# Optimization experiments

Hardware: AMD Instinct MI355X
Metric: run time of the kernel (lower is better)

Reference implementation:

```python
import jax, jax.numpy as jnp
import numpy as np

N = 100000   # nodes
E = 600000   # edges
B = 512      # graphs in batch
H = 128      # hidden dim
ED = 8       # edge feature dim
TWO48 = float(2 ** 48 - 1)


def _w(k, shape, fan_in):
    return jax.random.normal(k, shape, jnp.float32) * (1.0 / np.sqrt(fan_in))


def setup_inputs() -> dict:
    key = jax.random.key(0)
    ks = jax.random.split(key, 32)
    inp = {}
    inp["s_node_ids"] = jax.random.randint(ks[0], (N,), 0, 2 ** 31 - 1, dtype=jnp.int32)
    inp["s_edge_index"] = jax.random.randint(ks[1], (2, E), 0, N, dtype=jnp.int32)
    inp["s_edge_attr"] = jax.random.normal(ks[2], (E, ED), jnp.float32)
    inp["s_batch"] = jnp.sort(jax.random.randint(ks[3], (N,), 0, B, dtype=jnp.int32))
    inp["depth"] = jax.random.uniform(ks[4], (B,), jnp.float32)
    # id_mlp: Linear(1,H) -> ReLU -> Linear(H,H)
    inp["id_w1"] = _w(ks[5], (1, H), 1); inp["id_b1"] = jnp.zeros((H,), jnp.float32)
    inp["id_w2"] = _w(ks[6], (H, H), H); inp["id_b2"] = jnp.zeros((H,), jnp.float32)
    # edge_mlp: Linear(ED,H) -> ReLU -> Linear(H,H)
    inp["ed_w1"] = _w(ks[7], (ED, H), ED); inp["ed_b1"] = jnp.zeros((H,), jnp.float32)
    inp["ed_w2"] = _w(ks[8], (H, H), H); inp["ed_b2"] = jnp.zeros((H,), jnp.float32)
    # GINEConv nn MLPs: Linear(H,H) -> ReLU -> Linear(H,H)
    inp["c1_w1"] = _w(ks[9], (H, H), H); inp["c1_b1"] = jnp.zeros((H,), jnp.float32)
    inp["c1_w2"] = _w(ks[10], (H, H), H); inp["c1_b2"] = jnp.zeros((H,), jnp.float32)
    inp["c2_w1"] = _w(ks[11], (H, H), H); inp["c2_b1"] = jnp.zeros((H,), jnp.float32)
    inp["c2_w2"] = _w(ks[12], (H, H), H); inp["c2_b2"] = jnp.zeros((H,), jnp.float32)
    inp["rg_w1"] = _w(ks[13], (H + 1, H), H + 1); inp["rg_b1"] = jnp.zeros((H,), jnp.float32)
    inp["rg_w2"] = _w(ks[14], (H, 1), H); inp["rg_b2"] = jnp.zeros((1,), jnp.float32)
    return inp


def _mlp2(x, w1, b1, w2, b2):
    return jax.nn.relu(x @ w1 + b1) @ w2 + b2


def _gine(x, src, dst, e, w1, b1, w2, b2):
    # message = ReLU(x_j + e), sum-aggregated at dst; out = nn((1+eps)*x + aggr), eps=0
    msg = jax.nn.relu(x[src] + e)                       # [E, H]
    aggr = jax.ops.segment_sum(msg, dst, num_segments=N)  # [N, H]
    return _mlp2(x + aggr, w1, b1, w2, b2)


def _global_mean(x, batch):
    sums = jax.ops.segment_sum(x, batch, num_segments=B)                          # [B, H]
    cnts = jax.ops.segment_sum(jnp.ones((x.shape[0], 1), x.dtype), batch, num_segments=B)
    return sums / jnp.maximum(cnts, 1.0)


def reference(s_node_ids, s_edge_index, s_edge_attr, s_batch, depth,
              id_w1, id_b1, id_w2, id_b2,
              ed_w1, ed_b1, ed_w2, ed_b2,
              c1_w1, c1_b1, c1_w2, c1_b2,
              c2_w1, c2_b1, c2_w2, c2_b2,
              rg_w1, rg_b1, rg_w2, rg_b2):
    src, dst = s_edge_index[0], s_edge_index[1]
    x0 = jnp.clip(s_node_ids.astype(jnp.float32) / TWO48, 0.0, 1.0)[:, None]  # [N,1]
    x = _mlp2(x0, id_w1, id_b1, id_w2, id_b2)                                 # [N,H]
    e = _mlp2(s_edge_attr, ed_w1, ed_b1, ed_w2, ed_b2)                        # [E,H]
    x = jax.nn.relu(_gine(x, src, dst, e, c1_w1, c1_b1, c1_w2, c1_b2))
    x = jax.nn.relu(_gine(x, src, dst, e, c2_w1, c2_b1, c2_w2, c2_b2))
    rep = jnp.concatenate([_global_mean(x, s_batch), depth[:, None]], axis=1)  # [B,H+1]
    return _mlp2(rep, rg_w1, rg_b1, rg_w2, rg_b2)[:, 0]                        # [B]
```

## Files before the change

### kernel.cpp

```cpp
#include <hip/hip_runtime.h>
#include <hip/hip_bf16.h>

#define N_NODES 100000
#define N_EDGES 600000
#define NB      512
#define H       128
#define ED      8
#define SCAN_CHUNK 1024
#define N_CHUNKS   98

typedef __attribute__((ext_vector_type(8))) short short8;
typedef __attribute__((ext_vector_type(4))) float f32x4;
typedef __attribute__((ext_vector_type(4))) unsigned int u32x4;
typedef unsigned short u16;
typedef unsigned int   u32;

static __device__ __forceinline__ u16 f2bf(float f) {
    u32 u = __float_as_uint(f);
    u32 r = u + 0x7fffu + ((u >> 16) & 1u);
    return (u16)(r >> 16);
}
static __device__ __forceinline__ float bf2f(u32 h) {
    return __uint_as_float(h << 16);
}

__global__ __launch_bounds__(256) void pack_all_kernel(
    const float* __restrict__ W0, const float* __restrict__ W1,
    const float* __restrict__ W2, const float* __restrict__ W3,
    const float* __restrict__ W4, const float* __restrict__ W5,
    const float* __restrict__ W6,
    short8* __restrict__ O0, short8* __restrict__ O1,
    short8* __restrict__ O2, short8* __restrict__ O3,
    short8* __restrict__ O4, short8* __restrict__ O5,
    short8* __restrict__ O6)
{
    int gid = blockIdx.x * 256 + threadIdx.x;
    const int total = 512 + 6 * 2048;
    if (gid >= total) return;
    const float* W; short8* O; int Krows, kkmax, slot;
    if (gid < 512) { W = W0; O = O0; Krows = ED; kkmax = 1; slot = gid; }
    else {
        int m = (gid - 512) / 2048;
        slot = (gid - 512) % 2048;
        Krows = H; kkmax = 4;
        switch (m) {
            case 0: W = W1; O = O1; break;
            case 1: W = W2; O = O2; break;
            case 2: W = W3; O = O3; break;
            case 3: W = W4; O = O4; break;
            case 4: W = W5; O = O5; break;
            default: W = W6; O = O6; break;
        }
    }
    int lane = slot & 63;
    int t = slot >> 6;
    int nt = t & 1; t >>= 1;
    int kk = t % kkmax;
    int w  = t / kkmax;
    int quad = lane >> 4, n15 = lane & 15;
    int n = w * 32 + nt * 16 + n15;
    short8 v;
    #pragma unroll
    for (int j = 0; j < 8; j++) {
        int k = kk * 32 + quad * 8 + j;
        v[j] = (k < Krows) ? (short)f2bf(W[k * H + n]) : (short)0;
    }
    O[slot] = v;
}

__global__ __launch_bounds__(256) void hist_kernel(
    const int* __restrict__ edge_index, int* __restrict__ counts)
{
    int e = blockIdx.x * 256 + threadIdx.x;
    if (e < N_EDGES) atomicAdd(&counts[edge_index[N_EDGES + e]], 1);
}

__global__ __launch_bounds__(SCAN_CHUNK) void scan1_kernel(
    const int* __restrict__ counts, int* __restrict__ chunk_scan,
    int* __restrict__ bsum_raw)
{
    __shared__ int s[SCAN_CHUNK];
    int tid = threadIdx.x;
    int gid = blockIdx.x * SCAN_CHUNK + tid;
    int v = counts[gid];
    s[tid] = v;
    __syncthreads();
    #pragma unroll
    for (int off = 1; off < SCAN_CHUNK; off <<= 1) {
        int t = (tid >= off) ? s[tid - off] : 0;
        __syncthreads();
        s[tid] += t;
        __syncthreads();
    }
    chunk_scan[gid] = s[tid] - v;
    if (tid == SCAN_CHUNK - 1) bsum_raw[blockIdx.x] = s[tid];
}

__global__ __launch_bounds__(128) void scan2_kernel(
    const int* __restrict__ bsum_raw, int* __restrict__ bsum_scan)
{
    __shared__ int s[128];
    int tid = threadIdx.x;
    int v = (tid < N_CHUNKS) ? bsum_raw[tid] : 0;
    s[tid] = v;
    __syncthreads();
    #pragma unroll
    for (int off = 1; off < 128; off <<= 1) {
        int t = (tid >= off) ? s[tid - off] : 0;
        __syncthreads();
        s[tid] += t;
        __syncthreads();
    }
    bsum_scan[tid] = s[tid] - v;
}

__global__ __launch_bounds__(256) void fill_kernel(
    const int* __restrict__ edge_index,
    const int* __restrict__ chunk_scan, const int* __restrict__ bsum_scan,
    int* __restrict__ counts, int* __restrict__ src_list,
    int* __restrict__ pos_of)
{
    int e = blockIdx.x * 256 + threadIdx.x;
    if (e >= N_EDGES) return;
    int src = edge_index[e];
    int dst = edge_index[N_EDGES + e];
    int slot = atomicAdd(&counts[dst], -1) - 1;
    int pos = chunk_scan[dst] + bsum_scan[dst >> 10] + slot;
    src_list[pos] = src;
    pos_of[e] = pos;
}

__global__ __launch_bounds__(256) void finalize_offsets(
    const int* __restrict__ chunk_scan, const int* __restrict__ bsum_scan,
    int* __restrict__ row_start)
{
    int i = blockIdx.x * 256 + threadIdx.x;
    if (i <= N_NODES) row_start[i] = chunk_scan[i] + bsum_scan[i >> 10];
}

__global__ __launch_bounds__(256) void node_mlp_mfma(
    const int* __restrict__ ids,
    const float* __restrict__ w1, const float* __restrict__ b1,
    const short8* __restrict__ pW2, const float* __restrict__ b2,
    u16* __restrict__ x_out)
{
    __shared__ u16 sH[64 * 136];
    __shared__ float s_x0[64];
    int tid = threadIdx.x;
    int w = tid >> 6, lane = tid & 63, quad = lane >> 4, n15 = lane & 15;
    short8 fW2[4][2];
    #pragma unroll
    for (int kk = 0; kk < 4; kk++) {
        fW2[kk][0] = pW2[((w * 4 + kk) * 2 + 0) * 64 + lane];
        fW2[kk][1] = pW2[((w * 4 + kk) * 2 + 1) * 64 + lane];
    }
    float rb2[2] = { b2[w * 32 + n15], b2[w * 32 + 16 + n15] };
    float w1c = w1[tid & 127], b1c = b1[tid & 127];
    const int ntile = (N_NODES + 63) / 64;
    for (int tile = blockIdx.x; tile < ntile; tile += gridDim.x) {
        int row0 = tile * 64;
        if (tid < 64) {
            int n = row0 + tid;
            float x0 = (n < N_NODES) ? (float)ids[n] / 281474976710655.0f : 0.0f;
            s_x0[tid] = fminf(fmaxf(x0, 0.0f), 1.0f);
        }
        __syncthreads();
        int half = tid >> 7, c = tid & 127;
        #pragma unroll 8
        for (int rr = 0; rr < 32; rr++) {
            int r = half + rr * 2;
            sH[r * 136 + c] = f2bf(fmaxf(s_x0[r] * w1c + b1c, 0.0f));
        }
        __syncthreads();
        f32x4 acc[4][2];
        #pragma unroll
        for (int s = 0; s < 4; s++) { acc[s][0] = (f32x4){0,0,0,0}; acc[s][1] = (f32x4){0,0,0,0}; }
        #pragma unroll
        for (int kk = 0; kk < 4; kk++) {
            #pragma unroll
            for (int s = 0; s < 4; s++) {
                short8 a = *(const short8*)&sH[(s * 16 + n15) * 136 + kk * 32 + quad * 8];
                acc[s][0] = __builtin_amdgcn_mfma_f32_16x16x32_bf16(a, fW2[kk][0], acc[s][0], 0, 0, 0);
                acc[s][1] = __builtin_amdgcn_mfma_f32_16x16x32_bf16(a, fW2[kk][1], acc[s][1], 0, 0, 0);
            }
        }
        __syncthreads();
        #pragma unroll
        for (int s = 0; s < 4; s++)
            #pragma unroll
            for (int nt = 0; nt < 2; nt++) {
                int col = w * 32 + nt * 16 + n15;
                #pragma unroll
                for (int reg = 0; reg < 4; reg++)
                    sH[(s * 16 + quad * 4 + reg) * 136 + col] =
                        f2bf(acc[s][nt][reg] + rb2[nt]);
            }
        __syncthreads();
        for (int idx = tid; idx < 64 * 16; idx += 256) {
            int r = idx >> 4, c8 = (idx & 15) << 3;
            int n = row0 + r;
            if (n < N_NODES)
                *(uint4*)&x_out[(long)n * H + c8] = *(const uint4*)&sH[r * 136 + c8];
        }
        __syncthreads();
    }
}

__global__ __launch_bounds__(256) void edge_mlp_mfma(
    const float* __restrict__ attr,
    const int* __restrict__ pos_of,
    const short8* __restrict__ pW1, const float* __restrict__ b1,
    const short8* __restrict__ pW2, const float* __restrict__ b2,
    u16* __restrict__ e_perm)
{
    __shared__ u16 sA[64 * 40];
    __shared__ u16 sH[64 * 136];
    __shared__ int sPos[64];
    int tid = threadIdx.x;
    int w = tid >> 6, lane = tid & 63, quad = lane >> 4, n15 = lane & 15;
    short8 fW1[2];
    fW1[0] = pW1[(w * 2 + 0) * 64 + lane];
    fW1[1] = pW1[(w * 2 + 1) * 64 + lane];
    short8 fW2[4][2];
    #pragma unroll
    for (int kk = 0; kk < 4; kk++) {
        fW2[kk][0] = pW2[((w * 4 + kk) * 2 + 0) * 64 + lane];
        fW2[kk][1] = pW2[((w * 4 + kk) * 2 + 1) * 64 + lane];
    }
    float rb1[2] = { b1[w * 32 + n15], b1[w * 32 + 16 + n15] };
    float rb2[2] = { b2[w * 32 + n15], b2[w * 32 + 16 + n15] };
    const int ntile = N_EDGES / 64;
    for (int tile = blockIdx.x; tile < ntile; tile += gridDim.x) {
        int row0 = tile * 64;
        if (tid < 64) sPos[tid] = pos_of[row0 + tid];
        if (tid >= 64 && tid < 192) {
            int t2 = tid - 64;
            int r = t2 >> 1, c4 = (t2 & 1) * 4;
            f32x4 v = __builtin_nontemporal_load((const f32x4*)&attr[(long)(row0 + r) * ED + c4]);
            ushort4 o;
            o.x = f2bf(v[0]); o.y = f2bf(v[1]); o.z = f2bf(v[2]); o.w = f2bf(v[3]);
            *(ushort4*)&sA[r * 40 + c4] = o;
        } else if (tid >= 192) {
            int idx = tid - 192;
            for (; idx < 192; idx += 64) {
                int r = idx / 3, c8 = 8 + (idx % 3) * 8;
                *(uint4*)&sA[r * 40 + c8] = make_uint4(0, 0, 0, 0);
            }
        }
        __syncthreads();
        f32x4 acc[4][2];
        #pragma unroll
        for (int s = 0; s < 4; s++) { acc[s][0] = (f32x4){0,0,0,0}; acc[s][1] = (f32x4){0,0,0,0}; }
        #pragma unroll
        for (int s = 0; s < 4; s++) {
            short8 a = *(const short8*)&sA[(s * 16 + n15) * 40 + quad * 8];
            acc[s][0] = __builtin_amdgcn_mfma_f32_16x16x32_bf16(a, fW1[0], acc[s][0], 0, 0, 0);
            acc[s][1] = __builtin_amdgcn_mfma_f32_16x16x32_bf16(a, fW1[1], acc[s][1], 0, 0, 0);
        }
        #pragma unroll
        for (int s = 0; s < 4; s++)
            #pragma unroll
            for (int nt = 0; nt < 2; nt++) {
                int col = w * 32 + nt * 16 + n15;
                #pragma unroll
                for (int reg = 0; reg < 4; reg++)
                    sH[(s * 16 + quad * 4 + reg) * 136 + col] =
                        f2bf(fmaxf(acc[s][nt][reg] + rb1[nt], 0.0f));
            }
        __syncthreads();
        #pragma unroll
        for (int s = 0; s < 4; s++) { acc[s][0] = (f32x4){0,0,0,0}; acc[s][1] = (f32x4){0,0,0,0}; }
        #pragma unroll
        for (int kk = 0; kk < 4; kk++) {
            #pragma unroll
            for (int s = 0; s < 4; s++) {
                short8 a = *(const short8*)&sH[(s * 16 + n15) * 136 + kk * 32 + quad * 8];
                acc[s][0] = __builtin_amdgcn_mfma_f32_16x16x32_bf16(a, fW2[kk][0], acc[s][0], 0, 0, 0);
                acc[s][1] = __builtin_amdgcn_mfma_f32_16x16x32_bf16(a, fW2[kk][1], acc[s][1], 0, 0, 0);
            }
        }
        __syncthreads();
        #pragma unroll
        for (int s = 0; s < 4; s++)
            #pragma unroll
            for (int nt = 0; nt < 2; nt++) {
                int col = w * 32 + nt * 16 + n15;
                #pragma unroll
                for (int reg = 0; reg < 4; reg++)
                    sH[(s * 16 + quad * 4 + reg) * 136 + col] =
                        f2bf(acc[s][nt][reg] + rb2[nt]);
            }
        __syncthreads();
        for (int idx = tid; idx < 64 * 16; idx += 256) {
            int r = idx >> 4, c8 = (idx & 15) << 3;
            long rr = sPos[r];
            u32x4 v = *(const u32x4*)&sH[r * 136 + c8];
            __builtin_nontemporal_store(v, (u32x4*)&e_perm[rr * H + c8]);
        }
        __syncthreads();
    }
}

static __device__ __forceinline__ void acc8(float* a, u32x4 xv, u32x4 ev) {
    #pragma unroll
    for (int q = 0; q < 4; q++) {
        a[2 * q + 0] += fmaxf(bf2f(xv[q] & 0xffff) + bf2f(ev[q] & 0xffff), 0.0f);
        a[2 * q + 1] += fmaxf(bf2f(xv[q] >> 16)    + bf2f(ev[q] >> 16),    0.0f);
    }
}

__global__ __launch_bounds__(256) void aggregate_kernel(
    const int* __restrict__ row_start,
    const int* __restrict__ src_list,
    const u16* __restrict__ e_perm,
    const u16* __restrict__ x,
    u16* __restrict__ xs_out)
{
    int tid  = threadIdx.x;
    int lane = tid & 63;
    int l16  = lane & 15;
    int base = lane & 48;
    int fo   = l16 * 8;
    int n = blockIdx.x * 16 + (tid >> 4);
    const u16* xb = x + fo;

    int beg = row_start[n];
    int end = row_start[n + 1];
    float a[8], b[8];
    #pragma unroll
    for (int q = 0; q < 8; q++) { a[q] = 0.0f; b[q] = 0.0f; }

    for (int j0 = beg; j0 < end; j0 += 16) {
        int m = min(16, end - j0);
        int sv = src_list[j0 + min(l16, m - 1)];
        const u16* ej = e_perm + (long)j0 * H + fo;
        int j = 0;
        for (; j + 2 <= m; j += 2) {
            int s0 = __shfl(sv, base | j);
            int s1 = __shfl(sv, base | (j + 1));
            u32x4 xv0 = *(const u32x4*)(xb + (long)s0 * H);
            u32x4 ev0 = __builtin_nontemporal_load((const u32x4*)(ej + (long)(j + 0) * H));
            u32x4 xv1 = *(const u32x4*)(xb + (long)s1 * H);
            u32x4 ev1 = __builtin_nontemporal_load((const u32x4*)(ej + (long)(j + 1) * H));
            acc8(a, xv0, ev0);
            acc8(b, xv1, ev1);
        }
        if (j < m) {
            int s0 = __shfl(sv, base | j);
            u32x4 xv0 = *(const u32x4*)(xb + (long)s0 * H);
            u32x4 ev0 = __builtin_nontemporal_load((const u32x4*)(ej + (long)j * H));
            acc8(a, xv0, ev0);
        }
    }
    u32x4 xself = *(const u32x4*)(xb + (long)n * H);
    u32x4 out;
    #pragma unroll
    for (int q = 0; q < 4; q++) {
        float o0 = bf2f(xself[q] & 0xffff) + a[2 * q + 0] + b[2 * q + 0];
        float o1 = bf2f(xself[q] >> 16)    + a[2 * q + 1] + b[2 * q + 1];
        out[q] = (u32)f2bf(o0) | ((u32)f2bf(o1) << 16);
    }
    __builtin_nontemporal_store(out, (u32x4*)&xs_out[(long)n * H + fo]);
}

__global__ __launch_bounds__(256) void conv_mlp_mfma(
    const u16* __restrict__ xs,
    const short8* __restrict__ pW1, const float* __restrict__ b1,
    const short8* __restrict__ pW2, const float* __restrict__ b2,
    u16* __restrict__ x_out)
{
    __shared__ u16 sA[32 * 136];
    int tid = threadIdx.x;
    int w = tid >> 6, lane = tid & 63, quad = lane >> 4, n15 = lane & 15;
    short8 fW1[4][2], fW2[4][2];
    #pragma unroll
    for (int kk = 0; kk < 4; kk++) {
        fW1[kk][0] = pW1[((w * 4 + kk) * 2 + 0) * 64 + lane];
        fW1[kk][1] = pW1[((w * 4 + kk) * 2 + 1) * 64 + lane];
        fW2[kk][0] = pW2[((w * 4 + kk) * 2 + 0) * 64 + lane];
        fW2[kk][1] = pW2[((w * 4 + kk) * 2 + 1) * 64 + lane];
    }
    float rb1[2] = { b1[w * 32 + n15], b1[w * 32 + 16 + n15] };
    float rb2[2] = { b2[w * 32 + n15], b2[w * 32 + 16 + n15] };
    const int ntile = N_NODES / 32;
    for (int tile = blockIdx.x; tile < ntile; tile += gridDim.x) {
        long row0 = (long)tile * 32;
        for (int idx = tid; idx < 32 * 16; idx += 256) {
            int r = idx >> 4, c8 = (idx & 15) << 3;
            *(uint4*)&sA[r * 136 + c8] = *(const uint4*)&xs[(row0 + r) * H + c8];
        }
        __syncthreads();
        f32x4 acc[2][2];
        #pragma unroll
        for (int s = 0; s < 2; s++) { acc[s][0] = (f32x4){0,0,0,0}; acc[s][1] = (f32x4){0,0,0,0}; }
        #pragma unroll
        for (int kk = 0; kk < 4; kk++) {
            #pragma unroll
            for (int s = 0; s < 2; s++) {
                short8 a = *(const short8*)&sA[(s * 16 + n15) * 136 + kk * 32 + quad * 8];
                acc[s][0] = __builtin_amdgcn_mfma_f32_16x16x32_bf16(a, fW1[kk][0], acc[s][0], 0, 0, 0);
                acc[s][1] = __builtin_amdgcn_mfma_f32_16x16x32_bf16(a, fW1[kk][1], acc[s][1], 0, 0, 0);
            }
        }
        __syncthreads();
        #pragma unroll
        for (int s = 0; s < 2; s++)
            #pragma unroll
            for (int nt = 0; nt < 2; nt++) {
                int col = w * 32 + nt * 16 + n15;
                #pragma unroll
                for (int reg = 0; reg < 4; reg++)
                    sA[(s * 16 + quad * 4 + reg) * 136 + col] =
                        f2bf(fmaxf(acc[s][nt][reg] + rb1[nt], 0.0f));
            }
        __syncthreads();
        #pragma unroll
        for (int s = 0; s < 2; s++) { acc[s][0] = (f32x4){0,0,0,0}; acc[s][1] = (f32x4){0,0,0,0}; }
        #pragma unroll
        for (int kk = 0; kk < 4; kk++) {
            #pragma unroll
            for (int s = 0; s < 2; s++) {
                short8 a = *(const short8*)&sA[(s * 16 + n15) * 136 + kk * 32 + quad * 8];
                acc[s][0] = __builtin_amdgcn_mfma_f32_16x16x32_bf16(a, fW2[kk][0], acc[s][0], 0, 0, 0);
                acc[s][1] = __builtin_amdgcn_mfma_f32_16x16x32_bf16(a, fW2[kk][1], acc[s][1], 0, 0, 0);
            }
        }
        __syncthreads();
        #pragma unroll
        for (int s = 0; s < 2; s++)
            #pragma unroll
            for (int nt = 0; nt < 2; nt++) {
                int col = w * 32 + nt * 16 + n15;
                #pragma unroll
                for (int reg = 0; reg < 4; reg++)
                    sA[(s * 16 + quad * 4 + reg) * 136 + col] =
                        f2bf(fmaxf(acc[s][nt][reg] + rb2[nt], 0.0f));
            }
        __syncthreads();
        for (int idx = tid; idx < 32 * 16; idx += 256) {
            int r = idx >> 4, c8 = (idx & 15) << 3;
            *(uint4*)&x_out[(row0 + r) * H + c8] = *(const uint4*)&sA[r * 136 + c8];
        }
        __syncthreads();
    }
}

__global__ __launch_bounds__(256) void pool_kernel(
    const u16* __restrict__ x, const int* __restrict__ batch,
    float* __restrict__ sums, float* __restrict__ cnt)
{
    int sg   = threadIdx.x >> 6;
    int lane = threadIdx.x & 63;
    int fo = lane * 2;
    const int nper = (N_NODES + gridDim.x - 1) / gridDim.x;
    int n0 = blockIdx.x * nper;
    int n1 = min(n0 + nper, N_NODES);
    int cur = -1;
    float a0 = 0.0f, a1 = 0.0f, c = 0.0f;
    for (int n = n0 + sg; n < n1; n += 4) {
        int b = batch[n];
        if (b != cur) {
            if (cur >= 0) {
                atomicAdd(&sums[cur * H + fo],     a0);
                atomicAdd(&sums[cur * H + fo + 1], a1);
                if (lane == 0) atomicAdd(&cnt[cur], c);
            }
            a0 = a1 = 0.0f; c = 0.0f; cur = b;
        }
        u32 xv = *(const u32*)&x[(long)n * H + fo];
        a0 += bf2f(xv & 0xffff);
        a1 += bf2f(xv >> 16);
        c += 1.0f;
    }
    if (cur >= 0) {
        atomicAdd(&sums[cur * H + fo],     a0);
        atomicAdd(&sums[cur * H + fo + 1], a1);
        if (lane == 0) atomicAdd(&cnt[cur], c);
    }
}

__global__ __launch_bounds__(128) void regressor_kernel(
    const float* __restrict__ sums, const float* __restrict__ cnt,
    const float* __restrict__ depth,
    const float* __restrict__ w1, const float* __restrict__ b1,
    const float* __restrict__ w2, const float* __restrict__ b2,
    float* __restrict__ out)
{
    __shared__ float s_mean[H];
    __shared__ float s_red[2];
    int b = blockIdx.x;
    int j = threadIdx.x;
    float c = fmaxf(cnt[b], 1.0f);
    s_mean[j] = sums[b * H + j] / c;
    __syncthreads();
    float h = b1[j];
    #pragma unroll 8
    for (int k = 0; k < H; k++) h += s_mean[k] * w1[k * H + j];
    h += depth[b] * w1[H * H + j];
    h = fmaxf(h, 0.0f);
    float p = h * w2[j];
    #pragma unroll
    for (int off = 32; off >= 1; off >>= 1) p += __shfl_down(p, off, 64);
    if ((j & 63) == 0) s_red[j >> 6] = p;
    __syncthreads();
    if (j == 0) out[b] = s_red[0] + s_red[1] + b2[0];
}

extern "C" void kernel_launch(void* const* d_in, const int* in_sizes, int n_in,
                              void* d_out, int out_size, void* d_ws, size_t ws_size,
                              hipStream_t stream)
{
    const int*   ids   = (const int*)  d_in[0];
    const int*   eidx  = (const int*)  d_in[1];
    const float* eattr = (const float*)d_in[2];
    const int*   batch = (const int*)  d_in[3];
    const float* depth = (const float*)d_in[4];
    const float* id_w1 = (const float*)d_in[5];
    const float* id_b1 = (const float*)d_in[6];
    const float* id_w2 = (const float*)d_in[7];
    const float* id_b2 = (const float*)d_in[8];
    const float* ed_w1 = (const float*)d_in[9];
    const float* ed_b1 = (const float*)d_in[10];
    const float* ed_w2 = (const float*)d_in[11];
    const float* ed_b2 = (const float*)d_in[12];
    const float* c1_w1 = (const float*)d_in[13];
    const float* c1_b1 = (const float*)d_in[14];
    const float* c1_w2 = (const float*)d_in[15];
    const float* c1_b2 = (const float*)d_in[16];
    const float* c2_w1 = (const float*)d_in[17];
    const float* c2_b1 = (const float*)d_in[18];
    const float* c2_w2 = (const float*)d_in[19];
    const float* c2_b2 = (const float*)d_in[20];
    const float* rg_w1 = (const float*)d_in[21];
    const float* rg_b1 = (const float*)d_in[22];
    const float* rg_w2 = (const float*)d_in[23];
    const float* rg_b2 = (const float*)d_in[24];

    char* ws = (char*)d_ws;
    u16*   e_buf    = (u16*)  (ws);
    u16*   x_buf    = (u16*)  (ws + 153600000);
    u16*   xs_buf   = (u16*)  (ws + 179200000);
    float* sums_buf = (float*)(ws + 204800000);
    float* cnt_buf  = (float*)(ws + 205062144);
    int*   counts   = (int*)  (ws + 205064192);
    int*   chunk_sc = (int*)  (ws + 205465600);
    int*   bsum_raw = (int*)  (ws + 205867008);
    int*   bsum_sc  = (int*)  (ws + 205867520);
    int*   src_list = (int*)  (ws + 205868032);
    int*   pos_of   = (int*)  (ws + 208268032);
    short8* ed_w1p  = (short8*)(ws + 210668032);
    short8* ed_w2p  = (short8*)(ws + 210676224);
    short8* c1_w1p  = (short8*)(ws + 210708992);
    short8* c1_w2p  = (short8*)(ws + 210741760);
    short8* c2_w1p  = (short8*)(ws + 210774528);
    short8* c2_w2p  = (short8*)(ws + 210807296);
    short8* id_w2p  = (short8*)(ws + 210840064);
    int*   row_start = counts;

    pack_all_kernel<<<50, 256, 0, stream>>>(
        ed_w1, ed_w2, c1_w1, c1_w2, c2_w1, c2_w2, id_w2,
        ed_w1p, ed_w2p, c1_w1p, c1_w2p, c2_w1p, c2_w2p, id_w2p);

    hipMemsetAsync(counts, 0, 401408, stream);
    hist_kernel <<<(N_EDGES + 255) / 256, 256, 0, stream>>>(eidx, counts);
    scan1_kernel<<<N_CHUNKS, SCAN_CHUNK, 0, stream>>>(counts, chunk_sc, bsum_raw);
    scan2_kernel<<<1, 128, 0, stream>>>(bsum_raw, bsum_sc);
    fill_kernel <<<(N_EDGES + 255) / 256, 256, 0, stream>>>(eidx, chunk_sc, bsum_sc,
                                                            counts, src_list, pos_of);
    finalize_offsets<<<(N_NODES + 256) / 256, 256, 0, stream>>>(chunk_sc, bsum_sc, row_start);

    node_mlp_mfma<<<768, 256, 0, stream>>>(ids, id_w1, id_b1, id_w2p, id_b2, x_buf);
    edge_mlp_mfma<<<2048, 256, 0, stream>>>(eattr, pos_of, ed_w1p, ed_b1, ed_w2p, ed_b2, e_buf);

    aggregate_kernel<<<6250, 256, 0, stream>>>(row_start, src_list, e_buf, x_buf, xs_buf);
    conv_mlp_mfma<<<3125, 256, 0, stream>>>(xs_buf, c1_w1p, c1_b1, c1_w2p, c1_b2, x_buf);

    aggregate_kernel<<<6250, 256, 0, stream>>>(row_start, src_list, e_buf, x_buf, xs_buf);
    conv_mlp_mfma<<<3125, 256, 0, stream>>>(xs_buf, c2_w1p, c2_b1, c2_w2p, c2_b2, x_buf);

    hipMemsetAsync(sums_buf, 0, (size_t)(NB * H + NB) * 4, stream);
    pool_kernel<<<2048, 256, 0, stream>>>(x_buf, batch, sums_buf, cnt_buf);
    regressor_kernel<<<NB, 128, 0, stream>>>(sums_buf, cnt_buf, depth,
                                             rg_w1, rg_b1, rg_w2, rg_b2, (float*)d_out);
}
```

Before: 408.1 us.

## Fuse edge MLP into GINE aggregation, recompute edge embeddings per layer

Removes the materialized 600k x 128 bf16 edge-embedding buffer. The fill kernel now writes bf16 edge attributes permuted into CSR order, and a new fused kernel recomputes the edge MLP with MFMA for each CSR chunk of 64 edges. Each block handles 32 destination nodes and accumulates relu(x_src + e) directly from LDS. This trades roughly 150MB of write-then-double-read traffic for running the edge MLP twice. It also cuts parallelism: each thread now serially walks the edges of two nodes, and tiles can be partially filled.

```diff
diff --git a/kernel.cpp b/kernel.cpp
--- a/kernel.cpp
+++ b/kernel.cpp
@@ -118,7 +118,7 @@
     const int* __restrict__ edge_index,
     const int* __restrict__ chunk_scan, const int* __restrict__ bsum_scan,
     int* __restrict__ counts, int* __restrict__ src_list,
-    int* __restrict__ pos_of)
+    const float* __restrict__ attr, u16* __restrict__ attr_perm)
 {
     int e = blockIdx.x * 256 + threadIdx.x;
     if (e >= N_EDGES) return;
@@ -127,7 +127,13 @@
     int slot = atomicAdd(&counts[dst], -1) - 1;
     int pos = chunk_scan[dst] + bsum_scan[dst >> 10] + slot;
     src_list[pos] = src;
-    pos_of[e] = pos;
+    float4 v0 = *(const float4*)&attr[(long)e * ED];
+    float4 v1 = *(const float4*)&attr[(long)e * ED + 4];
+    u32 w0 = (u32)f2bf(v0.x) | ((u32)f2bf(v0.y) << 16);
+    u32 w1 = (u32)f2bf(v0.z) | ((u32)f2bf(v0.w) << 16);
+    u32 w2 = (u32)f2bf(v1.x) | ((u32)f2bf(v1.y) << 16);
+    u32 w3 = (u32)f2bf(v1.z) | ((u32)f2bf(v1.w) << 16);
+    *(uint4*)&attr_perm[(long)pos * ED] = make_uint4(w0, w1, w2, w3);
 }
 
 __global__ __launch_bounds__(256) void finalize_offsets(
@@ -206,16 +212,18 @@
     }
 }
 
-__global__ __launch_bounds__(256) void edge_mlp_mfma(
-    const float* __restrict__ attr,
-    const int* __restrict__ pos_of,
+__global__ __launch_bounds__(256) void gine_msg_fused(
+    const int* __restrict__ row_start,
+    const int* __restrict__ src_list,
+    const u16* __restrict__ attr_perm,
+    const u16* __restrict__ x,
     const short8* __restrict__ pW1, const float* __restrict__ b1,
     const short8* __restrict__ pW2, const float* __restrict__ b2,
-    u16* __restrict__ e_perm)
+    u16* __restrict__ xs_out)
 {
     __shared__ u16 sA[64 * 40];
     __shared__ u16 sH[64 * 136];
-    __shared__ int sPos[64];
+    __shared__ int sSrc[64];
     int tid = threadIdx.x;
     int w = tid >> 6, lane = tid & 63, quad = lane >> 4, n15 = lane & 15;
     short8 fW1[2];
@@ -229,23 +237,32 @@
     }
     float rb1[2] = { b1[w * 32 + n15], b1[w * 32 + 16 + n15] };
     float rb2[2] = { b2[w * 32 + n15], b2[w * 32 + 16 + n15] };
-    const int ntile = N_EDGES / 64;
-    for (int tile = blockIdx.x; tile < ntile; tile += gridDim.x) {
-        int row0 = tile * 64;
-        if (tid < 64) sPos[tid] = pos_of[row0 + tid];
-        if (tid >= 64 && tid < 192) {
-            int t2 = tid - 64;
-            int r = t2 >> 1, c4 = (t2 & 1) * 4;
-            f32x4 v = __builtin_nontemporal_load((const f32x4*)&attr[(long)(row0 + r) * ED + c4]);
-            ushort4 o;
-            o.x = f2bf(v[0]); o.y = f2bf(v[1]); o.z = f2bf(v[2]); o.w = f2bf(v[3]);
-            *(ushort4*)&sA[r * 40 + c4] = o;
-        } else if (tid >= 192) {
-            int idx = tid - 192;
-            for (; idx < 192; idx += 64) {
-                int r = idx / 3, c8 = 8 + (idx % 3) * 8;
-                *(uint4*)&sA[r * 40 + c8] = make_uint4(0, 0, 0, 0);
-            }
+    for (int idx = tid; idx < 64 * 3; idx += 256) {
+        int r = idx / 3, c8 = 8 + (idx % 3) * 8;
+        *(uint4*)&sA[r * 40 + c8] = make_uint4(0, 0, 0, 0);
+    }
+    int gid = tid >> 4, l16 = tid & 15, fo = l16 * 8;
+    int nd0 = blockIdx.x * 32;
+    int nA   = nd0 + gid * 2;
+    int begA = row_start[nA];
+    int endA = row_start[nA + 1];
+    int endB = row_start[nA + 2];
+    int p0   = row_start[nd0];
+    int pEnd = row_start[nd0 + 32];
+    const u16* xb = x + fo;
+    float a[8], b[8];
+    #pragma unroll
+    for (int q = 0; q < 8; q++) { a[q] = 0.0f; b[q] = 0.0f; }
+
+    for (int c0 = p0; c0 < pEnd; c0 += 64) {
+        int cnt = min(64, pEnd - c0);
+        int ce  = c0 + cnt;
+        if (tid < 64) {
+            if (tid < cnt) sSrc[tid] = src_list[c0 + tid];
+        } else if (tid < 128) {
+            int r = tid - 64;
+            if (r < cnt)
+                *(uint4*)&sA[r * 40] = *(const uint4*)&attr_perm[(long)(c0 + r) * ED];
         }
         __syncthreads();
         f32x4 acc[4][2];
@@ -253,9 +270,9 @@
         for (int s = 0; s < 4; s++) { acc[s][0] = (f32x4){0,0,0,0}; acc[s][1] = (f32x4){0,0,0,0}; }
         #pragma unroll
         for (int s = 0; s < 4; s++) {
-            short8 a = *(const short8*)&sA[(s * 16 + n15) * 40 + quad * 8];
-            acc[s][0] = __builtin_amdgcn_mfma_f32_16x16x32_bf16(a, fW1[0], acc[s][0], 0, 0, 0);
-            acc[s][1] = __builtin_amdgcn_mfma_f32_16x16x32_bf16(a, fW1[1], acc[s][1], 0, 0, 0);
+            short8 av = *(const short8*)&sA[(s * 16 + n15) * 40 + quad * 8];
+            acc[s][0] = __builtin_amdgcn_mfma_f32_16x16x32_bf16(av, fW1[0], acc[s][0], 0, 0, 0);
+            acc[s][1] = __builtin_amdgcn_mfma_f32_16x16x32_bf16(av, fW1[1], acc[s][1], 0, 0, 0);
         }
         #pragma unroll
         for (int s = 0; s < 4; s++)
@@ -274,9 +291,9 @@
         for (int kk = 0; kk < 4; kk++) {
             #pragma unroll
             for (int s = 0; s < 4; s++) {
-                short8 a = *(const short8*)&sH[(s * 16 + n15) * 136 + kk * 32 + quad * 8];
-                acc[s][0] = __builtin_amdgcn_mfma_f32_16x16x32_bf16(a, fW2[kk][0], acc[s][0], 0, 0, 0);
-                acc[s][1] = __builtin_amdgcn_mfma_f32_16x16x32_bf16(a, fW2[kk][1], acc[s][1], 0, 0, 0);
+                short8 av = *(const short8*)&sH[(s * 16 + n15) * 136 + kk * 32 + quad * 8];
+                acc[s][0] = __builtin_amdgcn_mfma_f32_16x16x32_bf16(av, fW2[kk][0], acc[s][0], 0, 0, 0);
+                acc[s][1] = __builtin_amdgcn_mfma_f32_16x16x32_bf16(av, fW2[kk][1], acc[s][1], 0, 0, 0);
             }
         }
         __syncthreads();
@@ -291,76 +308,54 @@
                         f2bf(acc[s][nt][reg] + rb2[nt]);
             }
         __syncthreads();
-        for (int idx = tid; idx < 64 * 16; idx += 256) {
-            int r = idx >> 4, c8 = (idx & 15) << 3;
-            long rr = sPos[r];
-            u32x4 v = *(const u32x4*)&sH[r * 136 + c8];
-            __builtin_nontemporal_store(v, (u32x4*)&e_perm[rr * H + c8]);
-        }
-        __syncthreads();
-    }
-}
-
-static __device__ __forceinline__ void acc8(float* a, u32x4 xv, u32x4 ev) {
+        {
+            int jb = max(begA, c0), je = min(endA, ce);
+            for (int j = jb; j < je; j++) {
+                int jl = j - c0;
+                int src = sSrc[jl];
+                u32x4 xv = *(const u32x4*)(xb + (long)src * H);
+                short8 ev = *(const short8*)&sH[jl * 136 + fo];
+                #pragma unroll
+                for (int q = 0; q < 8; q++) {
+                    float xf = bf2f((q & 1) ? (xv[q >> 1] >> 16) : (xv[q >> 1] & 0xffff));
+                    float ef = bf2f((u32)(unsigned short)ev[q]);
+                    a[q] += fmaxf(xf + ef, 0.0f);
+                }
+            }
+            jb = max(endA, c0); je = min(endB, ce);
+            for (int j = jb; j < je; j++) {
+                int jl = j - c0;
+                int src = sSrc[jl];
+                u32x4 xv = *(const u32x4*)(xb + (long)src * H);
+                short8 ev = *(const short8*)&sH[jl * 136 + fo];
+                #pragma unroll
+                for (int q = 0; q < 8; q++) {
+                    float xf = bf2f((q & 1) ? (xv[q >> 1] >> 16) : (xv[q >> 1] & 0xffff));
+                    float ef = bf2f((u32)(unsigned short)ev[q]);
+                    b[q] += fmaxf(xf + ef, 0.0f);
+                }
+            }
+        }
+        __syncthreads();
+    }
+    u32x4 xvA = *(const u32x4*)(xb + (long)nA * H);
+    u32x4 oA;
     #pragma unroll
     for (int q = 0; q < 4; q++) {
-        a[2 * q + 0] += fmaxf(bf2f(xv[q] & 0xffff) + bf2f(ev[q] & 0xffff), 0.0f);
-        a[2 * q + 1] += fmaxf(bf2f(xv[q] >> 16)    + bf2f(ev[q] >> 16),    0.0f);
-    }
-}
-
-__global__ __launch_bounds__(256) void aggregate_kernel(
-    const int* __restrict__ row_start,
-    const int* __restrict__ src_list,
-    const u16* __restrict__ e_perm,
-    const u16* __restrict__ x,
-    u16* __restrict__ xs_out)
-{
-    int tid  = threadIdx.x;
-    int lane = tid & 63;
-    int l16  = lane & 15;
-    int base = lane & 48;
-    int fo   = l16 * 8;
-    int n = blockIdx.x * 16 + (tid >> 4);
-    const u16* xb = x + fo;
-
-    int beg = row_start[n];
-    int end = row_start[n + 1];
-    float a[8], b[8];
-    #pragma unroll
-    for (int q = 0; q < 8; q++) { a[q] = 0.0f; b[q] = 0.0f; }
-
-    for (int j0 = beg; j0 < end; j0 += 16) {
-        int m = min(16, end - j0);
-        int sv = src_list[j0 + min(l16, m - 1)];
-        const u16* ej = e_perm + (long)j0 * H + fo;
-        int j = 0;
-        for (; j + 2 <= m; j += 2) {
-            int s0 = __shfl(sv, base | j);
-            int s1 = __shfl(sv, base | (j + 1));
-            u32x4 xv0 = *(const u32x4*)(xb + (long)s0 * H);
-            u32x4 ev0 = __builtin_nontemporal_load((const u32x4*)(ej + (long)(j + 0) * H));
-            u32x4 xv1 = *(const u32x4*)(xb + (long)s1 * H);
-            u32x4 ev1 = __builtin_nontemporal_load((const u32x4*)(ej + (long)(j + 1) * H));
-            acc8(a, xv0, ev0);
-            acc8(b, xv1, ev1);
-        }
-        if (j < m) {
-            int s0 = __shfl(sv, base | j);
-            u32x4 xv0 = *(const u32x4*)(xb + (long)s0 * H);
-            u32x4 ev0 = __builtin_nontemporal_load((const u32x4*)(ej + (long)j * H));
-            acc8(a, xv0, ev0);
-        }
-    }
-    u32x4 xself = *(const u32x4*)(xb + (long)n * H);
-    u32x4 out;
+        float o0 = bf2f(xvA[q] & 0xffff) + a[2 * q + 0];
+        float o1 = bf2f(xvA[q] >> 16)    + a[2 * q + 1];
+        oA[q] = (u32)f2bf(o0) | ((u32)f2bf(o1) << 16);
+    }
+    *(u32x4*)&xs_out[(long)nA * H + fo] = oA;
+    u32x4 xvB = *(const u32x4*)(xb + (long)(nA + 1) * H);
+    u32x4 oB;
     #pragma unroll
     for (int q = 0; q < 4; q++) {
-        float o0 = bf2f(xself[q] & 0xffff) + a[2 * q + 0] + b[2 * q + 0];
-        float o1 = bf2f(xself[q] >> 16)    + a[2 * q + 1] + b[2 * q + 1];
-        out[q] = (u32)f2bf(o0) | ((u32)f2bf(o1) << 16);
-    }
-    __builtin_nontemporal_store(out, (u32x4*)&xs_out[(long)n * H + fo]);
+        float o0 = bf2f(xvB[q] & 0xffff) + b[2 * q + 0];
+        float o1 = bf2f(xvB[q] >> 16)    + b[2 * q + 1];
+        oB[q] = (u32)f2bf(o0) | ((u32)f2bf(o1) << 16);
+    }
+    *(u32x4*)&xs_out[(long)(nA + 1) * H + fo] = oB;
 }
 
 __global__ __launch_bounds__(256) void conv_mlp_mfma(
@@ -537,24 +532,23 @@
     const float* rg_b2 = (const float*)d_in[24];
 
     char* ws = (char*)d_ws;
-    u16*   e_buf    = (u16*)  (ws);
-    u16*   x_buf    = (u16*)  (ws + 153600000);
-    u16*   xs_buf   = (u16*)  (ws + 179200000);
-    float* sums_buf = (float*)(ws + 204800000);
-    float* cnt_buf  = (float*)(ws + 205062144);
-    int*   counts   = (int*)  (ws + 205064192);
-    int*   chunk_sc = (int*)  (ws + 205465600);
-    int*   bsum_raw = (int*)  (ws + 205867008);
-    int*   bsum_sc  = (int*)  (ws + 205867520);
-    int*   src_list = (int*)  (ws + 205868032);
-    int*   pos_of   = (int*)  (ws + 208268032);
-    short8* ed_w1p  = (short8*)(ws + 210668032);
-    short8* ed_w2p  = (short8*)(ws + 210676224);
-    short8* c1_w1p  = (short8*)(ws + 210708992);
-    short8* c1_w2p  = (short8*)(ws + 210741760);
-    short8* c2_w1p  = (short8*)(ws + 210774528);
-    short8* c2_w2p  = (short8*)(ws + 210807296);
-    short8* id_w2p  = (short8*)(ws + 210840064);
+    u16*   attr_perm = (u16*) (ws);
+    u16*   x_buf    = (u16*)  (ws + 9600000);
+    u16*   xs_buf   = (u16*)  (ws + 35200000);
+    float* sums_buf = (float*)(ws + 60800000);
+    float* cnt_buf  = (float*)(ws + 61062144);
+    int*   counts   = (int*)  (ws + 61064192);
+    int*   chunk_sc = (int*)  (ws + 61465600);
+    int*   bsum_raw = (int*)  (ws + 61867008);
+    int*   bsum_sc  = (int*)  (ws + 61867520);
+    int*   src_list = (int*)  (ws + 61868032);
+    short8* ed_w1p  = (short8*)(ws + 64268032);
+    short8* ed_w2p  = (short8*)(ws + 64276224);
+    short8* c1_w1p  = (short8*)(ws + 64308992);
+    short8* c1_w2p  = (short8*)(ws + 64341760);
+    short8* c2_w1p  = (short8*)(ws + 64374528);
+    short8* c2_w2p  = (short8*)(ws + 64407296);
+    short8* id_w2p  = (short8*)(ws + 64440064);
     int*   row_start = counts;
 
     pack_all_kernel<<<50, 256, 0, stream>>>(
@@ -566,16 +560,18 @@
     scan1_kernel<<<N_CHUNKS, SCAN_CHUNK, 0, stream>>>(counts, chunk_sc, bsum_raw);
     scan2_kernel<<<1, 128, 0, stream>>>(bsum_raw, bsum_sc);
     fill_kernel <<<(N_EDGES + 255) / 256, 256, 0, stream>>>(eidx, chunk_sc, bsum_sc,
-                                                            counts, src_list, pos_of);
+                                                            counts, src_list,
+                                                            eattr, attr_perm);
     finalize_offsets<<<(N_NODES + 256) / 256, 256, 0, stream>>>(chunk_sc, bsum_sc, row_start);
 
     node_mlp_mfma<<<768, 256, 0, stream>>>(ids, id_w1, id_b1, id_w2p, id_b2, x_buf);
-    edge_mlp_mfma<<<2048, 256, 0, stream>>>(eattr, pos_of, ed_w1p, ed_b1, ed_w2p, ed_b2, e_buf);
-
-    aggregate_kernel<<<6250, 256, 0, stream>>>(row_start, src_list, e_buf, x_buf, xs_buf);
+
+    gine_msg_fused<<<3125, 256, 0, stream>>>(row_start, src_list, attr_perm, x_buf,
+                                             ed_w1p, ed_b1, ed_w2p, ed_b2, xs_buf);
     conv_mlp_mfma<<<3125, 256, 0, stream>>>(xs_buf, c1_w1p, c1_b1, c1_w2p, c1_b2, x_buf);
 
-    aggregate_kernel<<<6250, 256, 0, stream>>>(row_start, src_list, e_buf, x_buf, xs_buf);
+    gine_msg_fused<<<3125, 256, 0, stream>>>(row_start, src_list, attr_perm, x_buf,
+                                             ed_w1p, ed_b1, ed_w2p, ed_b2, xs_buf);
     conv_mlp_mfma<<<3125, 256, 0, stream>>>(xs_buf, c2_w1p, c2_b1, c2_w2p, c2_b2, x_buf);
 
     hipMemsetAsync(sums_buf, 0, (size_t)(NB * H + NB) * 4, stream);
```

Measured after the change: 567.5 us. 39.1% more time.
